# Optimization experiments

Measured on AMD Instinct MI355X. Metric: run time of the kernel, lower is better.

Reference implementation:

```python
import jax, jax.numpy as jnp
import numpy as np

D_MODEL = 256
NHEAD = 8
D_FF = 2 * D_MODEL
N_LAYERS = 4
LAYER_NAMES = ("self", "cross", "self", "cross")
EPS_ATTN = 1e-6
EPS_LN = 1e-5


def pos_encoding(x):
    # LoFTR-style 2D sinusoidal positional encoding, x: [N, C, H, W]
    n, c, h, w = x.shape
    d4 = c // 4
    # exp(arange(0, c//2, 2) * (-log(1e4) / (c//2)))
    div = jnp.exp(jnp.arange(d4, dtype=jnp.float32) * 2.0 * (-np.log(10000.0) / (c // 2)))
    xs = jnp.arange(w, dtype=jnp.float32)[None, None, :]   # [1,1,W]
    ys = jnp.arange(h, dtype=jnp.float32)[None, :, None]   # [1,H,1]
    dv = div[:, None, None]                                 # [d4,1,1]
    sx = jnp.broadcast_to(jnp.sin(xs * dv), (d4, h, w))
    cx = jnp.broadcast_to(jnp.cos(xs * dv), (d4, h, w))
    sy = jnp.broadcast_to(jnp.sin(ys * dv), (d4, h, w))
    cy = jnp.broadcast_to(jnp.cos(ys * dv), (d4, h, w))
    pe = jnp.stack([sx, cx, sy, cy], axis=1).reshape(c, h, w)  # channel order pe[0::4]=sin_x,...
    return x + pe[None]


def linear_attention(q, k, v):
    # q: [N,L,H,d], k/v: [N,S,H,d]
    Q = jax.nn.elu(q) + 1.0
    K = jax.nn.elu(k) + 1.0
    KV = jnp.einsum('nshd,nshm->nhmd', K, v)                 # [N,H,d,d]
    Z = 1.0 / (jnp.einsum('nlhd,nhd->nlh', Q, K.sum(axis=1)) + EPS_ATTN)
    return jnp.einsum('nlhd,nhmd,nlh->nlhm', Q, KV, Z)       # [N,L,H,d]


def layer_norm(x, g, b):
    m = jnp.mean(x, axis=-1, keepdims=True)
    v = jnp.mean(jnp.square(x - m), axis=-1, keepdims=True)
    return (x - m) / jnp.sqrt(v + EPS_LN) * g + b


def encoder_layer(x, src, p):
    N, L, _ = x.shape
    q = (x @ p['Wq'] + p['bq']).reshape(N, L, NHEAD, -1)
    S = src.shape[1]
    k = (src @ p['Wk'] + p['bk']).reshape(N, S, NHEAD, -1)
    v = (src @ p['Wv'] + p['bv']).reshape(N, S, NHEAD, -1)
    attn = linear_attention(q, k, v).reshape(N, L, -1) @ p['Wo'] + p['bo']
    x = layer_norm(x + attn, p['g1'], p['be1'])
    y = jax.nn.relu(x @ p['W1'] + p['b1']) @ p['W2'] + p['b2']
    return layer_norm(x + y, p['g2'], p['be2'])


def _params_at(i, Wq, bq, Wk, bk, Wv, bv, Wo, bo, W1, b1, W2, b2, g1, be1, g2, be2):
    return dict(Wq=Wq[i], bq=bq[i], Wk=Wk[i], bk=bk[i], Wv=Wv[i], bv=bv[i],
                Wo=Wo[i], bo=bo[i], W1=W1[i], b1=b1[i], W2=W2[i], b2=b2[i],
                g1=g1[i], be1=be1[i], g2=g2[i], be2=be2[i])


def setup_inputs() -> dict:
    key = jax.random.key(0)
    ks = jax.random.split(key, 16)
    N, C, H, W = 4, D_MODEL, 64, 64
    d, dff, Ln = D_MODEL, D_FF, N_LAYERS
    s = 1.0 / np.sqrt(d)
    sf = 1.0 / np.sqrt(dff)
    return {
        'ref_feature': jax.random.normal(ks[0], (N, C, H, W), jnp.float32),
        'src_feature': jax.random.normal(ks[1], (N, C, H, W), jnp.float32),
        'Wq': jax.random.normal(ks[2], (Ln, d, d), jnp.float32) * s,
        'bq': jnp.zeros((Ln, d), jnp.float32),
        'Wk': jax.random.normal(ks[3], (Ln, d, d), jnp.float32) * s,
        'bk': jnp.zeros((Ln, d), jnp.float32),
        'Wv': jax.random.normal(ks[4], (Ln, d, d), jnp.float32) * s,
        'bv': jnp.zeros((Ln, d), jnp.float32),
        'Wo': jax.random.normal(ks[5], (Ln, d, d), jnp.float32) * s,
        'bo': jnp.zeros((Ln, d), jnp.float32),
        'W1': jax.random.normal(ks[6], (Ln, d, dff), jnp.float32) * s,
        'b1': jnp.zeros((Ln, dff), jnp.float32),
        'W2': jax.random.normal(ks[7], (Ln, dff, d), jnp.float32) * sf,
        'b2': jnp.zeros((Ln, d), jnp.float32),
        'g1': jnp.ones((Ln, d), jnp.float32),
        'be1': jnp.zeros((Ln, d), jnp.float32),
        'g2': jnp.ones((Ln, d), jnp.float32),
        'be2': jnp.zeros((Ln, d), jnp.float32),
    }


def reference(ref_feature, src_feature, Wq, bq, Wk, bk, Wv, bv, Wo, bo,
              W1, b1, W2, b2, g1, be1, g2, be2):
    # FMT.forward(feat='cross')
    N, C, H, W = ref_feature.shape
    f0 = pos_encoding(ref_feature).transpose(0, 2, 3, 1).reshape(N, H * W, C)
    f1 = pos_encoding(src_feature).transpose(0, 2, 3, 1).reshape(N, H * W, C)
    p1 = jnp.concatenate([f0, f1], axis=0)   # [2N, L, C]
    p2 = jnp.concatenate([f1, f0], axis=0)
    for i, name in enumerate(LAYER_NAMES):
        p = _params_at(i, Wq, bq, Wk, bk, Wv, bv, Wo, bo, W1, b1, W2, b2, g1, be1, g2, be2)
        src = p1 if name == 'self' else p2
        p1 = encoder_layer(p1, src, p)
    out = p1.reshape(2 * N, H, W, C).transpose(0, 3, 1, 2)  # [2N, C, H, W]
    return out
```

## Files before the change

### kernel.cpp

```cpp
#include <hip/hip_runtime.h>
#include <hip/hip_bf16.h>

typedef __bf16 bf16;
typedef __attribute__((ext_vector_type(8))) __bf16 bf16x8;
typedef __attribute__((ext_vector_type(4))) __bf16 bf16x4;
typedef __attribute__((ext_vector_type(4))) float f32x4;

__device__ __forceinline__ bf16 f2bf(float f) { return (bf16)f; }

__device__ __forceinline__ void async_cp16(const void* g, void* l) {
    __builtin_amdgcn_global_load_lds(
        (const __attribute__((address_space(1))) unsigned int*)g,
        (__attribute__((address_space(3))) unsigned int*)l, 16, 0, 0);
}

__device__ __forceinline__ float pe_val(int c, int t) {
    int h = t >> 6, w = t & 63;
    int i = c >> 2, j = c & 3;
    float div = expf(-0.14391156831212787f * (float)i);
    float arg = ((j < 2) ? (float)w : (float)h) * div;
    return (j & 1) ? cosf(arg) : sinf(arg);
}

__global__ __launch_bounds__(1024) void encode_kernel(const float* __restrict__ ref,
                                                      const float* __restrict__ src,
                                                      bf16* __restrict__ Xb,
                                                      bf16* __restrict__ P2b) {
    __shared__ float tile[32][33];
    int n = blockIdx.z >> 1, sel = blockIdx.z & 1;
    const float* f = sel ? src : ref;
    int t = blockIdx.x * 32 + threadIdx.x;
    int c = blockIdx.y * 32 + threadIdx.y;
    float v = f[((size_t)n * 256 + c) * 4096 + t] + pe_val(c, t);
    tile[threadIdx.y][threadIdx.x] = v;
    __syncthreads();
    int tt = blockIdx.x * 32 + threadIdx.y;
    int cc = blockIdx.y * 32 + threadIdx.x;
    float o = tile[threadIdx.x][threadIdx.y];
    int bx = sel ? 4 + n : n;
    int bp = sel ? n : 4 + n;
    Xb [((size_t)bx * 4096 + tt) * 256 + cc] = f2bf(o);
    P2b[((size_t)bp * 4096 + tt) * 256 + cc] = f2bf(o);
}

__global__ __launch_bounds__(1024) void wt_conv(const float* __restrict__ Wq, const float* __restrict__ Wk,
                                                const float* __restrict__ Wv, const float* __restrict__ Wo,
                                                const float* __restrict__ W1, const float* __restrict__ W2,
                                                bf16* __restrict__ Wt) {
    __shared__ float t[32][33];
    int z = blockIdx.z, L = z / 6, m = z - L * 6;
    const float* src; int K, N, doff;
    if      (m == 0) { src = Wq + L * 65536;  K = 256; N = 256; doff = 0; }
    else if (m == 1) { src = Wk + L * 65536;  K = 256; N = 256; doff = 65536; }
    else if (m == 2) { src = Wv + L * 65536;  K = 256; N = 256; doff = 131072; }
    else if (m == 3) { src = Wo + L * 65536;  K = 256; N = 256; doff = 196608; }
    else if (m == 4) { src = W1 + L * 131072; K = 256; N = 512; doff = 262144; }
    else             { src = W2 + L * 131072; K = 512; N = 256; doff = 393216; }
    int n0 = blockIdx.x * 32, k0 = blockIdx.y * 32;
    if (n0 >= N || k0 >= K) return;
    t[threadIdx.y][threadIdx.x] = src[(size_t)(k0 + threadIdx.y) * N + n0 + threadIdx.x];
    __syncthreads();
    bf16* dst = Wt + (size_t)L * 524288 + doff;
    dst[(size_t)(n0 + threadIdx.y) * K + k0 + threadIdx.x] = f2bf(t[threadIdx.x][threadIdx.y]);
}

__global__ __launch_bounds__(256) void gemm_qkv(const bf16* __restrict__ Aq,
                                                const bf16* __restrict__ Akv,
                                                const bf16* __restrict__ Wt,
                                                const float* __restrict__ bq,
                                                const float* __restrict__ bk,
                                                const float* __restrict__ bv,
                                                bf16* __restrict__ Q,
                                                bf16* __restrict__ Ko,
                                                bf16* __restrict__ V) {
    __shared__ bf16 Als[128 * 64];
    __shared__ bf16 Bls[128 * 64];
    int tid = threadIdx.x;
    int wave = tid >> 6, lane = tid & 63;
    int bm = blockIdx.y * 128, bn = blockIdx.x * 128;
    int wm = (wave >> 1) * 64, wn = (wave & 1) * 64;
    int l15 = lane & 15, g = lane >> 4;
    const int K = 256;

    int seg = bn >> 8, cloc = bn & 255;
    const bf16* A = seg == 0 ? Aq : Akv;
    const float* bias = seg == 0 ? bq : (seg == 1 ? bk : bv);
    bf16* Out = seg == 0 ? Q : (seg == 1 ? Ko : V);
    bool do_elu = seg < 2;

    f32x4 acc[4][4] = {};

    for (int k0 = 0; k0 < K; k0 += 64) {
#pragma unroll
        for (int r = 0; r < 4; ++r) {
            int Lc = r * 256 + tid;
            int row = Lc >> 3, cs = Lc & 7;
            int gc = cs ^ (row & 7);
            async_cp16(A  + (size_t)(bm + row) * K + k0 + gc * 8, &Als[Lc * 8]);
            async_cp16(Wt + (size_t)(bn + row) * K + k0 + gc * 8, &Bls[Lc * 8]);
        }
        __syncthreads();
#pragma unroll
        for (int ks = 0; ks < 2; ++ks) {
            bf16x8 af[4], bfr[4];
#pragma unroll
            for (int i = 0; i < 4; ++i) {
                int row = wm + i * 16 + l15;
                int c = ks * 4 + g;
                af[i] = *(bf16x8*)&Als[row * 64 + ((c ^ (row & 7)) * 8)];
            }
#pragma unroll
            for (int j = 0; j < 4; ++j) {
                int row = wn + j * 16 + l15;
                int c = ks * 4 + g;
                bfr[j] = *(bf16x8*)&Bls[row * 64 + ((c ^ (row & 7)) * 8)];
            }
#pragma unroll
            for (int i = 0; i < 4; ++i)
#pragma unroll
                for (int j = 0; j < 4; ++j)
                    acc[i][j] = __builtin_amdgcn_mfma_f32_16x16x32_bf16(af[i], bfr[j], acc[i][j], 0, 0, 0);
        }
        __syncthreads();
    }

    int r4 = (lane >> 4) * 4;
#pragma unroll
    for (int i = 0; i < 4; ++i) {
#pragma unroll
        for (int j = 0; j < 4; ++j) {
            int cj = cloc + wn + j * 16 + l15;
            float bvv = bias[cj];
#pragma unroll
            for (int r = 0; r < 4; ++r) {
                int row = bm + wm + i * 16 + r4 + r;
                float v = acc[i][j][r] + bvv;
                if (do_elu) v = v > 0.f ? v + 1.f : expf(v);
                Out[(size_t)row * 256 + cj] = f2bf(v);
            }
        }
    }
}

template <int RELU>
__global__ __launch_bounds__(256) void gemm_mfma(const bf16* __restrict__ A,
                                                 const bf16* __restrict__ Wt,
                                                 const float* __restrict__ bias,
                                                 bf16* __restrict__ C,
                                                 int N, int K) {
    __shared__ bf16 Als[128 * 64];
    __shared__ bf16 Bls[128 * 64];
    int tid = threadIdx.x;
    int wave = tid >> 6, lane = tid & 63;
    int bm = blockIdx.y * 128, bn = blockIdx.x * 128;
    int wm = (wave >> 1) * 64, wn = (wave & 1) * 64;
    int l15 = lane & 15, g = lane >> 4;

    f32x4 acc[4][4] = {};

    for (int k0 = 0; k0 < K; k0 += 64) {
#pragma unroll
        for (int r = 0; r < 4; ++r) {
            int Lc = r * 256 + tid;
            int row = Lc >> 3, cs = Lc & 7;
            int gc = cs ^ (row & 7);
            async_cp16(A  + (size_t)(bm + row) * K + k0 + gc * 8, &Als[Lc * 8]);
            async_cp16(Wt + (size_t)(bn + row) * K + k0 + gc * 8, &Bls[Lc * 8]);
        }
        __syncthreads();
#pragma unroll
        for (int ks = 0; ks < 2; ++ks) {
            bf16x8 af[4], bfr[4];
#pragma unroll
            for (int i = 0; i < 4; ++i) {
                int row = wm + i * 16 + l15;
                int c = ks * 4 + g;
                af[i] = *(bf16x8*)&Als[row * 64 + ((c ^ (row & 7)) * 8)];
            }
#pragma unroll
            for (int j = 0; j < 4; ++j) {
                int row = wn + j * 16 + l15;
                int c = ks * 4 + g;
                bfr[j] = *(bf16x8*)&Bls[row * 64 + ((c ^ (row & 7)) * 8)];
            }
#pragma unroll
            for (int i = 0; i < 4; ++i)
#pragma unroll
                for (int j = 0; j < 4; ++j)
                    acc[i][j] = __builtin_amdgcn_mfma_f32_16x16x32_bf16(af[i], bfr[j], acc[i][j], 0, 0, 0);
        }
        __syncthreads();
    }

    int r4 = (lane >> 4) * 4;
#pragma unroll
    for (int i = 0; i < 4; ++i) {
#pragma unroll
        for (int j = 0; j < 4; ++j) {
            int col = bn + wn + j * 16 + l15;
            float bvv = bias[col];
#pragma unroll
            for (int r = 0; r < 4; ++r) {
                int row = bm + wm + i * 16 + r4 + r;
                float v = acc[i][j][r] + bvv;
                if (RELU) v = fmaxf(v, 0.f);
                C[(size_t)row * N + col] = f2bf(v);
            }
        }
    }
}

__global__ __launch_bounds__(512) void gemm_ln(const bf16* __restrict__ A,
                                               const bf16* __restrict__ Wt,
                                               const float* __restrict__ bias,
                                               bf16* __restrict__ Xb,
                                               const float* __restrict__ g,
                                               const float* __restrict__ b,
                                               int K) {
    __shared__ __align__(16) char smem[128 * 260 * 2];
    bf16* Als = (bf16*)smem;
    bf16* Bls = (bf16*)(smem + 16384);
    bf16* Cls = (bf16*)smem;

    int tid = threadIdx.x;
    int wave = tid >> 6, lane = tid & 63;
    int bm = blockIdx.x * 128;
    int wm = (wave >> 2) * 64, wn = (wave & 3) * 64;
    int l15 = lane & 15, gg = lane >> 4;

    f32x4 acc[4][4] = {};

    for (int k0 = 0; k0 < K; k0 += 64) {
#pragma unroll
        for (int r = 0; r < 2; ++r) {
            int Lc = r * 512 + tid;
            int row = Lc >> 3, cs = Lc & 7;
            int gc = cs ^ (row & 7);
            async_cp16(A + (size_t)(bm + row) * K + k0 + gc * 8, &Als[Lc * 8]);
        }
#pragma unroll
        for (int r = 0; r < 4; ++r) {
            int Lc = r * 512 + tid;
            int row = Lc >> 3, cs = Lc & 7;
            int gc = cs ^ (row & 7);
            async_cp16(Wt + (size_t)row * K + k0 + gc * 8, &Bls[Lc * 8]);
        }
        __syncthreads();
#pragma unroll
        for (int ks = 0; ks < 2; ++ks) {
            bf16x8 af[4], bfr[4];
#pragma unroll
            for (int i = 0; i < 4; ++i) {
                int row = wm + i * 16 + l15;
                int c = ks * 4 + gg;
                af[i] = *(bf16x8*)&Als[row * 64 + ((c ^ (row & 7)) * 8)];
            }
#pragma unroll
            for (int j = 0; j < 4; ++j) {
                int row = wn + j * 16 + l15;
                int c = ks * 4 + gg;
                bfr[j] = *(bf16x8*)&Bls[row * 64 + ((c ^ (row & 7)) * 8)];
            }
#pragma unroll
            for (int i = 0; i < 4; ++i)
#pragma unroll
                for (int j = 0; j < 4; ++j)
                    acc[i][j] = __builtin_amdgcn_mfma_f32_16x16x32_bf16(af[i], bfr[j], acc[i][j], 0, 0, 0);
        }
        __syncthreads();
    }

    int r4 = (lane >> 4) * 4;
#pragma unroll
    for (int j = 0; j < 4; ++j) {
        int col = wn + j * 16 + l15;
        float bvv = bias[col];
#pragma unroll
        for (int i = 0; i < 4; ++i)
#pragma unroll
            for (int r = 0; r < 4; ++r)
                Cls[(wm + i * 16 + r4 + r) * 260 + col] = f2bf(acc[i][j][r] + bvv);
    }
    __syncthreads();

    int c4 = lane * 4;
    float4 gw = *(const float4*)&g[c4];
    float4 bw = *(const float4*)&b[c4];
#pragma unroll 2
    for (int rw = 0; rw < 16; ++rw) {
        int row = wave * 16 + rw;
        size_t gidx = (size_t)(bm + row) * 256 + c4;
        bf16x4 xb = *(const bf16x4*)(Xb + gidx);
        bf16x4 cb = *(const bf16x4*)&Cls[row * 260 + c4];
        float4 v;
        v.x = (float)xb[0] + (float)cb[0];
        v.y = (float)xb[1] + (float)cb[1];
        v.z = (float)xb[2] + (float)cb[2];
        v.w = (float)xb[3] + (float)cb[3];
        float s  = v.x + v.y + v.z + v.w;
        float sq = v.x * v.x + v.y * v.y + v.z * v.z + v.w * v.w;
#pragma unroll
        for (int off = 32; off > 0; off >>= 1) {
            s  += __shfl_xor(s,  off);
            sq += __shfl_xor(sq, off);
        }
        float mean = s * (1.f / 256.f);
        float var  = sq * (1.f / 256.f) - mean * mean;
        float rstd = rsqrtf(var + 1e-5f);
        bf16x4 ob;
        ob[0] = f2bf((v.x - mean) * rstd * gw.x + bw.x);
        ob[1] = f2bf((v.y - mean) * rstd * gw.y + bw.y);
        ob[2] = f2bf((v.z - mean) * rstd * gw.z + bw.z);
        ob[3] = f2bf((v.w - mean) * rstd * gw.w + bw.w);
        *(bf16x4*)(Xb + gidx) = ob;
    }
}

__global__ __launch_bounds__(512) void gemm_attn_ln(const bf16* __restrict__ A,
                                                    const float* __restrict__ Zt,
                                                    const bf16* __restrict__ Weff,
                                                    const float* __restrict__ bias,
                                                    bf16* __restrict__ Xb,
                                                    const float* __restrict__ g,
                                                    const float* __restrict__ b) {
    __shared__ __align__(16) char smem[128 * 260 * 2];
    bf16* Als = (bf16*)smem;
    bf16* Bls = (bf16*)(smem + 16384);
    bf16* Cls = (bf16*)smem;

    int tid = threadIdx.x;
    int wave = tid >> 6, lane = tid & 63;
    int bm = blockIdx.x * 128;
    const bf16* Wt = Weff + (size_t)(bm >> 12) * 65536;
    int wm = (wave >> 2) * 64, wn = (wave & 3) * 64;
    int l15 = lane & 15, gg = lane >> 4;

    f32x4 acc[4][4] = {};

    for (int k0 = 0; k0 < 256; k0 += 64) {
#pragma unroll
        for (int r = 0; r < 4; ++r) {
            int Lc = r * 512 + tid;
            int row = Lc >> 3, cs = Lc & 7;
            int gc = cs ^ (row & 7);
            async_cp16(Wt + (size_t)row * 256 + k0 + gc * 8, &Bls[Lc * 8]);
        }
#pragma unroll
        for (int r = 0; r < 2; ++r) {
            int Lc = r * 512 + tid;
            int row = Lc >> 3, cs = Lc & 7;
            int gc = cs ^ (row & 7);
            int gcol = k0 + gc * 8;
            bf16x8 q8 = *(const bf16x8*)(A + (size_t)(bm + row) * 256 + gcol);
            float z = Zt[(size_t)(bm + row) * 8 + (gcol >> 5)];
            bf16x8 a8;
#pragma unroll
            for (int u = 0; u < 8; ++u) a8[u] = f2bf((float)q8[u] * z);
            *(bf16x8*)&Als[Lc * 8] = a8;
        }
        __syncthreads();
#pragma unroll
        for (int ks = 0; ks < 2; ++ks) {
            bf16x8 af[4], bfr[4];
#pragma unroll
            for (int i = 0; i < 4; ++i) {
                int row = wm + i * 16 + l15;
                int c = ks * 4 + gg;
                af[i] = *(bf16x8*)&Als[row * 64 + ((c ^ (row & 7)) * 8)];
            }
#pragma unroll
            for (int j = 0; j < 4; ++j) {
                int row = wn + j * 16 + l15;
                int c = ks * 4 + gg;
                bfr[j] = *(bf16x8*)&Bls[row * 64 + ((c ^ (row & 7)) * 8)];
            }
#pragma unroll
            for (int i = 0; i < 4; ++i)
#pragma unroll
                for (int j = 0; j < 4; ++j)
                    acc[i][j] = __builtin_amdgcn_mfma_f32_16x16x32_bf16(af[i], bfr[j], acc[i][j], 0, 0, 0);
        }
        __syncthreads();
    }

    int r4 = (lane >> 4) * 4;
#pragma unroll
    for (int j = 0; j < 4; ++j) {
        int col = wn + j * 16 + l15;
        float bvv = bias[col];
#pragma unroll
        for (int i = 0; i < 4; ++i)
#pragma unroll
            for (int r = 0; r < 4; ++r)
                Cls[(wm + i * 16 + r4 + r) * 260 + col] = f2bf(acc[i][j][r] + bvv);
    }
    __syncthreads();

    int c4 = lane * 4;
    float4 gw = *(const float4*)&g[c4];
    float4 bw = *(const float4*)&b[c4];
#pragma unroll 2
    for (int rw = 0; rw < 16; ++rw) {
        int row = wave * 16 + rw;
        size_t gidx = (size_t)(bm + row) * 256 + c4;
        bf16x4 xb = *(const bf16x4*)(Xb + gidx);
        bf16x4 cb = *(const bf16x4*)&Cls[row * 260 + c4];
        float4 v;
        v.x = (float)xb[0] + (float)cb[0];
        v.y = (float)xb[1] + (float)cb[1];
        v.z = (float)xb[2] + (float)cb[2];
        v.w = (float)xb[3] + (float)cb[3];
        float s  = v.x + v.y + v.z + v.w;
        float sq = v.x * v.x + v.y * v.y + v.z * v.z + v.w * v.w;
#pragma unroll
        for (int off = 32; off > 0; off >>= 1) {
            s  += __shfl_xor(s,  off);
            sq += __shfl_xor(sq, off);
        }
        float mean = s * (1.f / 256.f);
        float var  = sq * (1.f / 256.f) - mean * mean;
        float rstd = rsqrtf(var + 1e-5f);
        bf16x4 ob;
        ob[0] = f2bf((v.x - mean) * rstd * gw.x + bw.x);
        ob[1] = f2bf((v.y - mean) * rstd * gw.y + bw.y);
        ob[2] = f2bf((v.z - mean) * rstd * gw.z + bw.z);
        ob[3] = f2bf((v.w - mean) * rstd * gw.w + bw.w);
        *(bf16x4*)(Xb + gidx) = ob;
    }
}

__global__ __launch_bounds__(256) void kv_prep_part(const bf16* __restrict__ Kb,
                                                    const bf16* __restrict__ Vb,
                                                    float* __restrict__ Pkv,
                                                    float* __restrict__ Pks) {
    __shared__ float Ks[128][32];
    __shared__ float Vs[128][32];
    int sp = blockIdx.x;
    int nh = blockIdx.y;
    int n = nh >> 3, h = nh & 7;
    int tid = threadIdx.x;
    int wave = tid >> 6, lane = tid & 63;
    int mg = lane >> 3;
    int dg = lane & 7;
    size_t base = ((size_t)n * 4096 + sp * 128) * 256 + h * 32;

#pragma unroll
    for (int p = 0; p < 2; ++p) {
        int r = p * 64 + (tid >> 2);
        int c = (tid & 3) * 8;
        bf16x8 k8 = *(const bf16x8*)(Kb + base + (size_t)r * 256 + c);
        bf16x8 v8 = *(const bf16x8*)(Vb + base + (size_t)r * 256 + c);
#pragma unroll
        for (int u = 0; u < 8; ++u) { Ks[r][c + u] = (float)k8[u]; Vs[r][c + u] = (float)v8[u]; }
    }
    __syncthreads();

    float acc[4][4] = {};
    float ks4[4] = {};
    int s0 = wave * 32;
    for (int s = s0; s < s0 + 32; ++s) {
        float4 kq = *(float4*)&Ks[s][dg * 4];
        float4 vq = *(float4*)&Vs[s][mg * 4];
        ks4[0] += kq.x; ks4[1] += kq.y; ks4[2] += kq.z; ks4[3] += kq.w;
        acc[0][0] += vq.x * kq.x; acc[0][1] += vq.x * kq.y; acc[0][2] += vq.x * kq.z; acc[0][3] += vq.x * kq.w;
        acc[1][0] += vq.y * kq.x; acc[1][1] += vq.y * kq.y; acc[1][2] += vq.y * kq.z; acc[1][3] += vq.y * kq.w;
        acc[2][0] += vq.z * kq.x; acc[2][1] += vq.z * kq.y; acc[2][2] += vq.z * kq.z; acc[2][3] += vq.z * kq.w;
        acc[3][0] += vq.w * kq.x; acc[3][1] += vq.w * kq.y; acc[3][2] += vq.w * kq.z; acc[3][3] += vq.w * kq.w;
    }
    __syncthreads();

    float* R  = &Ks[0][0];
    float* RS = &Vs[0][0];
#pragma unroll
    for (int mi = 0; mi < 4; ++mi)
#pragma unroll
        for (int dj = 0; dj < 4; ++dj)
            R[wave * 1024 + (mg * 4 + mi) * 32 + dg * 4 + dj] = acc[mi][dj];
    if (mg == 0)
#pragma unroll
        for (int dj = 0; dj < 4; ++dj) RS[wave * 32 + dg * 4 + dj] = ks4[dj];
    __syncthreads();

    int e = tid * 4;
    float4 o0 = *(float4*)&R[e];
    float4 o1 = *(float4*)&R[1024 + e];
    float4 o2 = *(float4*)&R[2048 + e];
    float4 o3 = *(float4*)&R[3072 + e];
    float4 o = make_float4(o0.x + o1.x + o2.x + o3.x, o0.y + o1.y + o2.y + o3.y,
                           o0.z + o1.z + o2.z + o3.z, o0.w + o1.w + o2.w + o3.w);
    *(float4*)&Pkv[((size_t)nh * 32 + sp) * 1024 + e] = o;
    if (tid < 32)
        Pks[((size_t)nh * 32 + sp) * 32 + tid] = RS[tid] + RS[32 + tid] + RS[64 + tid] + RS[96 + tid];
}

__global__ __launch_bounds__(64) void kv_reduce(const float* __restrict__ Pkv,
                                                const float* __restrict__ Pks,
                                                float* __restrict__ KV,
                                                float* __restrict__ Ksum) {
    int nh = blockIdx.x;
    int q = blockIdx.y;
    int e = (q * 64 + threadIdx.x) * 4;
    float4 s = make_float4(0.f, 0.f, 0.f, 0.f);
    for (int sp = 0; sp < 32; ++sp) {
        float4 p = *(const float4*)&Pkv[((size_t)nh * 32 + sp) * 1024 + e];
        s.x += p.x; s.y += p.y; s.z += p.z; s.w += p.w;
    }
    *(float4*)&KV[(size_t)nh * 1024 + e] = s;
    if (q == 0 && threadIdx.x < 32) {
        float ss = 0.f;
        for (int sp = 0; sp < 32; ++sp) ss += Pks[((size_t)nh * 32 + sp) * 32 + threadIdx.x];
        Ksum[nh * 32 + threadIdx.x] = ss;
    }
}

__global__ __launch_bounds__(256) void weff_kernel(const float* __restrict__ KV,
                                                   const bf16* __restrict__ WtO,
                                                   bf16* __restrict__ Weff) {
    __shared__ float KVs[8][1024];
    int n = blockIdx.y, c0 = blockIdx.x * 64;
    int tid = threadIdx.x;
    const float* src = KV + (size_t)n * 8192;
    for (int i = tid; i < 2048; i += 256)
        *(float4*)&((float*)KVs)[i * 4] = *(const float4*)&src[i * 4];
    __syncthreads();

    int c = c0 + (tid & 63);
    int hb = tid >> 6;
    const bf16* wrow = WtO + (size_t)c * 256 + hb * 64;
    bf16* dst = Weff + (size_t)n * 65536 + (size_t)c * 256 + hb * 64;

#pragma unroll
    for (int hh = 0; hh < 2; ++hh) {
        int h = hb * 2 + hh;
        float wo[32];
#pragma unroll
        for (int u = 0; u < 4; ++u) {
            bf16x8 w8 = *(const bf16x8*)(wrow + hh * 32 + u * 8);
#pragma unroll
            for (int v = 0; v < 8; ++v) wo[u * 8 + v] = (float)w8[v];
        }
        float s[32] = {};
        for (int m = 0; m < 32; ++m) {
            float wm = wo[m];
#pragma unroll
            for (int d4 = 0; d4 < 8; ++d4) {
                float4 kv4 = *(float4*)&KVs[h][m * 32 + d4 * 4];
                s[d4 * 4 + 0] += wm * kv4.x;
                s[d4 * 4 + 1] += wm * kv4.y;
                s[d4 * 4 + 2] += wm * kv4.z;
                s[d4 * 4 + 3] += wm * kv4.w;
            }
        }
#pragma unroll
        for (int u = 0; u < 4; ++u) {
            bf16x8 o8;
#pragma unroll
            for (int v = 0; v < 8; ++v) o8[v] = f2bf(s[u * 8 + v]);
            *(bf16x8*)(dst + hh * 32 + u * 8) = o8;
        }
    }
}

__global__ __launch_bounds__(256) void zcalc(const bf16* __restrict__ Qb,
                                             const float* __restrict__ Ksum,
                                             float* __restrict__ Zt) {
    int row = blockIdx.x * 4 + (threadIdx.x >> 6);
    int lane = threadIdx.x & 63;
    int n = row >> 12;
    int c = lane * 4;
    bf16x4 q = *(const bf16x4*)(Qb + (size_t)row * 256 + c);
    float4 k = *(const float4*)&Ksum[n * 256 + c];
    float s = (float)q[0] * k.x + (float)q[1] * k.y + (float)q[2] * k.z + (float)q[3] * k.w;
    s += __shfl_xor(s, 1); s += __shfl_xor(s, 2); s += __shfl_xor(s, 4);
    if ((lane & 7) == 0)
        Zt[(size_t)row * 8 + (lane >> 3)] = 1.f / (s + 1e-6f);
}

__global__ __launch_bounds__(1024) void store_kernel(const bf16* __restrict__ Xb,
                                                     float* __restrict__ out) {
    __shared__ float tile[32][33];
    int b = blockIdx.z;
    int t0 = blockIdx.x * 32, c0 = blockIdx.y * 32;
    tile[threadIdx.y][threadIdx.x] =
        (float)Xb[((size_t)b * 4096 + t0 + threadIdx.y) * 256 + c0 + threadIdx.x];
    __syncthreads();
    out[((size_t)b * 256 + c0 + threadIdx.y) * 4096 + t0 + threadIdx.x] =
        tile[threadIdx.x][threadIdx.y];
}

extern "C" void kernel_launch(void* const* d_in, const int* in_sizes, int n_in,
                              void* d_out, int out_size, void* d_ws, size_t ws_size,
                              hipStream_t stream) {
    const float* ref  = (const float*)d_in[0];
    const float* srcf = (const float*)d_in[1];
    const float* Wq = (const float*)d_in[2];
    const float* bq = (const float*)d_in[3];
    const float* Wk = (const float*)d_in[4];
    const float* bk = (const float*)d_in[5];
    const float* Wv = (const float*)d_in[6];
    const float* bv = (const float*)d_in[7];
    const float* Wo = (const float*)d_in[8];
    const float* bo = (const float*)d_in[9];
    const float* W1 = (const float*)d_in[10];
    const float* b1 = (const float*)d_in[11];
    const float* W2 = (const float*)d_in[12];
    const float* b2 = (const float*)d_in[13];
    const float* g1 = (const float*)d_in[14];
    const float* be1 = (const float*)d_in[15];
    const float* g2 = (const float*)d_in[16];
    const float* be2 = (const float*)d_in[17];

    const size_t SZ = (size_t)8 * 4096 * 256;
    float* ws  = (float*)d_ws;
    float* KVb = ws;
    float* Ksb = KVb + 65536;
    float* Pkv = Ksb + 2048;
    float* Pks = Pkv + 2097152;
    bf16*  Wt  = (bf16*)(Pks + 65536);
    bf16*  Xb  = Wt + 2097152;
    bf16*  P2b = Xb + SZ;
    bf16*  Qb  = P2b + SZ;
    bf16*  Weffb = (bf16*)Pkv;
    float* Ztb   = Pkv + 262144;
    bf16*  Kb  = (bf16*)d_out;
    bf16*  Vb  = Kb + SZ;
    bf16*  Hb  = Kb;

    wt_conv<<<dim3(16, 16, 24), dim3(32, 32), 0, stream>>>(Wq, Wk, Wv, Wo, W1, W2, Wt);
    encode_kernel<<<dim3(128, 8, 8), dim3(32, 32), 0, stream>>>(ref, srcf, Xb, P2b);

    for (int L = 0; L < 4; ++L) {
        const bf16* WtL = Wt + (size_t)L * 524288;
        const bf16* Akv = (L & 1) ? P2b : Xb;
        gemm_qkv<<<dim3(6, 256), 256, 0, stream>>>(Xb, Akv, WtL,
                                                   bq + L * 256, bk + L * 256, bv + L * 256,
                                                   Qb, Kb, Vb);
        kv_prep_part<<<dim3(32, 64), 256, 0, stream>>>(Kb, Vb, Pkv, Pks);
        kv_reduce<<<dim3(64, 4), 64, 0, stream>>>(Pkv, Pks, KVb, Ksb);
        weff_kernel<<<dim3(4, 8), 256, 0, stream>>>(KVb, WtL + 196608, Weffb);
        zcalc<<<8192, 256, 0, stream>>>(Qb, Ksb, Ztb);
        gemm_attn_ln<<<256, 512, 0, stream>>>(Qb, Ztb, Weffb, bo + L * 256, Xb,
                                              g1 + L * 256, be1 + L * 256);
        gemm_mfma<1><<<dim3(4, 256), 256, 0, stream>>>(Xb, WtL + 262144, b1 + L * 512, Hb, 512, 256);
        gemm_ln<<<256, 512, 0, stream>>>(Hb, WtL + 393216, b2 + L * 256, Xb,
                                         g2 + L * 256, be2 + L * 256, 512);
    }

    store_kernel<<<dim3(128, 8, 8), dim3(32, 32), 0, stream>>>(Xb, (float*)d_out);
}
```

Before: 683.6 us.

## Double-buffer LDS tiles and XCD-swizzle block order in QKV and FFN1 GEMMs

Both the QKV GEMM and the first FFN GEMM now use two LDS buffers, issuing the async global-to-LDS copy for the next K tile before computing on the current one. This is meant to overlap load latency with MFMA work. Launches switch to a 1D grid whose block index is remapped so consecutive tiles land on the same XCD, aiming for better L2 reuse of the A and B tiles. LDS use per block doubles to 64KB, which may cut occupancy, and only one barrier per iteration guards the buffer swap.

```diff
diff --git a/kernel.cpp b/kernel.cpp
--- a/kernel.cpp
+++ b/kernel.cpp
@@ -73,11 +73,13 @@
                                                 bf16* __restrict__ Q,
                                                 bf16* __restrict__ Ko,
                                                 bf16* __restrict__ V) {
-    __shared__ bf16 Als[128 * 64];
-    __shared__ bf16 Bls[128 * 64];
+    __shared__ bf16 Als[2][128 * 64];
+    __shared__ bf16 Bls[2][128 * 64];
     int tid = threadIdx.x;
     int wave = tid >> 6, lane = tid & 63;
-    int bm = blockIdx.y * 128, bn = blockIdx.x * 128;
+    int id = blockIdx.x;
+    int swz = (id & 7) * 192 + (id >> 3);
+    int bm = (swz / 6) * 128, bn = (swz % 6) * 128;
     int wm = (wave >> 1) * 64, wn = (wave & 1) * 64;
     int l15 = lane & 15, g = lane >> 4;
     const int K = 256;
@@ -90,16 +92,23 @@
 
     f32x4 acc[4][4] = {};
 
-    for (int k0 = 0; k0 < K; k0 += 64) {
-#pragma unroll
-        for (int r = 0; r < 4; ++r) {
-            int Lc = r * 256 + tid;
-            int row = Lc >> 3, cs = Lc & 7;
-            int gc = cs ^ (row & 7);
-            async_cp16(A  + (size_t)(bm + row) * K + k0 + gc * 8, &Als[Lc * 8]);
-            async_cp16(Wt + (size_t)(bn + row) * K + k0 + gc * 8, &Bls[Lc * 8]);
-        }
-        __syncthreads();
+#define QKV_STAGE(buf, k0)                                                      \
+    {                                                                           \
+        _Pragma("unroll")                                                       \
+        for (int r = 0; r < 4; ++r) {                                           \
+            int Lc = r * 256 + tid;                                             \
+            int row = Lc >> 3, cs = Lc & 7;                                     \
+            int gc = cs ^ (row & 7);                                            \
+            async_cp16(A  + (size_t)(bm + row) * K + (k0) + gc * 8, &Als[buf][Lc * 8]); \
+            async_cp16(Wt + (size_t)(bn + row) * K + (k0) + gc * 8, &Bls[buf][Lc * 8]); \
+        }                                                                       \
+    }
+
+    QKV_STAGE(0, 0);
+    __syncthreads();
+    int cur = 0;
+    for (int t = 0; t < 4; ++t) {
+        if (t < 3) QKV_STAGE(cur ^ 1, (t + 1) * 64);
 #pragma unroll
         for (int ks = 0; ks < 2; ++ks) {
             bf16x8 af[4], bfr[4];
@@ -107,13 +116,13 @@
             for (int i = 0; i < 4; ++i) {
                 int row = wm + i * 16 + l15;
                 int c = ks * 4 + g;
-                af[i] = *(bf16x8*)&Als[row * 64 + ((c ^ (row & 7)) * 8)];
+                af[i] = *(bf16x8*)&Als[cur][row * 64 + ((c ^ (row & 7)) * 8)];
             }
 #pragma unroll
             for (int j = 0; j < 4; ++j) {
                 int row = wn + j * 16 + l15;
                 int c = ks * 4 + g;
-                bfr[j] = *(bf16x8*)&Bls[row * 64 + ((c ^ (row & 7)) * 8)];
+                bfr[j] = *(bf16x8*)&Bls[cur][row * 64 + ((c ^ (row & 7)) * 8)];
             }
 #pragma unroll
             for (int i = 0; i < 4; ++i)
@@ -122,7 +131,9 @@
                     acc[i][j] = __builtin_amdgcn_mfma_f32_16x16x32_bf16(af[i], bfr[j], acc[i][j], 0, 0, 0);
         }
         __syncthreads();
-    }
+        cur ^= 1;
+    }
+#undef QKV_STAGE
 
     int r4 = (lane >> 4) * 4;
 #pragma unroll
@@ -147,27 +158,39 @@
                                                  const bf16* __restrict__ Wt,
                                                  const float* __restrict__ bias,
                                                  bf16* __restrict__ C,
-                                                 int N, int K) {
-    __shared__ bf16 Als[128 * 64];
-    __shared__ bf16 Bls[128 * 64];
+                                                 int N, int K, int nbn) {
+    __shared__ bf16 Als[2][128 * 64];
+    __shared__ bf16 Bls[2][128 * 64];
     int tid = threadIdx.x;
     int wave = tid >> 6, lane = tid & 63;
-    int bm = blockIdx.y * 128, bn = blockIdx.x * 128;
+    int id = blockIdx.x;
+    int nwg = gridDim.x;
+    int cpx = nwg >> 3;
+    int swz = (id & 7) * cpx + (id >> 3);
+    int bm = (swz / nbn) * 128, bn = (swz % nbn) * 128;
     int wm = (wave >> 1) * 64, wn = (wave & 1) * 64;
     int l15 = lane & 15, g = lane >> 4;
 
     f32x4 acc[4][4] = {};
 
-    for (int k0 = 0; k0 < K; k0 += 64) {
-#pragma unroll
-        for (int r = 0; r < 4; ++r) {
-            int Lc = r * 256 + tid;
-            int row = Lc >> 3, cs = Lc & 7;
-            int gc = cs ^ (row & 7);
-            async_cp16(A  + (size_t)(bm + row) * K + k0 + gc * 8, &Als[Lc * 8]);
-            async_cp16(Wt + (size_t)(bn + row) * K + k0 + gc * 8, &Bls[Lc * 8]);
-        }
-        __syncthreads();
+#define MF_STAGE(buf, k0)                                                       \
+    {                                                                           \
+        _Pragma("unroll")                                                       \
+        for (int r = 0; r < 4; ++r) {                                           \
+            int Lc = r * 256 + tid;                                             \
+            int row = Lc >> 3, cs = Lc & 7;                                     \
+            int gc = cs ^ (row & 7);                                            \
+            async_cp16(A  + (size_t)(bm + row) * K + (k0) + gc * 8, &Als[buf][Lc * 8]); \
+            async_cp16(Wt + (size_t)(bn + row) * K + (k0) + gc * 8, &Bls[buf][Lc * 8]); \
+        }                                                                       \
+    }
+
+    int nt = K >> 6;
+    MF_STAGE(0, 0);
+    __syncthreads();
+    int cur = 0;
+    for (int t = 0; t < nt; ++t) {
+        if (t < nt - 1) MF_STAGE(cur ^ 1, (t + 1) * 64);
 #pragma unroll
         for (int ks = 0; ks < 2; ++ks) {
             bf16x8 af[4], bfr[4];
@@ -175,13 +198,13 @@
             for (int i = 0; i < 4; ++i) {
                 int row = wm + i * 16 + l15;
                 int c = ks * 4 + g;
-                af[i] = *(bf16x8*)&Als[row * 64 + ((c ^ (row & 7)) * 8)];
+                af[i] = *(bf16x8*)&Als[cur][row * 64 + ((c ^ (row & 7)) * 8)];
             }
 #pragma unroll
             for (int j = 0; j < 4; ++j) {
                 int row = wn + j * 16 + l15;
                 int c = ks * 4 + g;
-                bfr[j] = *(bf16x8*)&Bls[row * 64 + ((c ^ (row & 7)) * 8)];
+                bfr[j] = *(bf16x8*)&Bls[cur][row * 64 + ((c ^ (row & 7)) * 8)];
             }
 #pragma unroll
             for (int i = 0; i < 4; ++i)
@@ -190,7 +213,9 @@
                     acc[i][j] = __builtin_amdgcn_mfma_f32_16x16x32_bf16(af[i], bfr[j], acc[i][j], 0, 0, 0);
         }
         __syncthreads();
-    }
+        cur ^= 1;
+    }
+#undef MF_STAGE
 
     int r4 = (lane >> 4) * 4;
 #pragma unroll
@@ -632,16 +657,16 @@
     for (int L = 0; L < 4; ++L) {
         const bf16* WtL = Wt + (size_t)L * 524288;
         const bf16* Akv = (L & 1) ? P2b : Xb;
-        gemm_qkv<<<dim3(6, 256), 256, 0, stream>>>(Xb, Akv, WtL,
-                                                   bq + L * 256, bk + L * 256, bv + L * 256,
-                                                   Qb, Kb, Vb);
+        gemm_qkv<<<1536, 256, 0, stream>>>(Xb, Akv, WtL,
+                                           bq + L * 256, bk + L * 256, bv + L * 256,
+                                           Qb, Kb, Vb);
         kv_prep_part<<<dim3(32, 64), 256, 0, stream>>>(Kb, Vb, Pkv, Pks);
         kv_reduce<<<dim3(64, 4), 64, 0, stream>>>(Pkv, Pks, KVb, Ksb);
         weff_kernel<<<dim3(4, 8), 256, 0, stream>>>(KVb, WtL + 196608, Weffb);
         zcalc<<<8192, 256, 0, stream>>>(Qb, Ksb, Ztb);
         gemm_attn_ln<<<256, 512, 0, stream>>>(Qb, Ztb, Weffb, bo + L * 256, Xb,
                                               g1 + L * 256, be1 + L * 256);
-        gemm_mfma<1><<<dim3(4, 256), 256, 0, stream>>>(Xb, WtL + 262144, b1 + L * 512, Hb, 512, 256);
+        gemm_mfma<1><<<1024, 256, 0, stream>>>(Xb, WtL + 262144, b1 + L * 512, Hb, 512, 256, 4);
         gemm_ln<<<256, 512, 0, stream>>>(Hb, WtL + 393216, b2 + L * 256, Xb,
                                          g2 + L * 256, be2 + L * 256, 512);
     }
```

New measurement: 674.6 us. Within noise of the previous version (-1.3%).
